# Kernel tuning notes

Hardware: AMD Instinct MI355X
Metric: run time of the kernel (lower is better)

Reference implementation:

```python
import jax, jax.numpy as jnp
import numpy as np

B, T, S, D = 8, 128, 512, 128  # batch, decoder steps, encoder len, output_dim==input_dim


def setup_inputs() -> dict:
    key = jax.random.key(0)
    ks = jax.random.split(key, 24)
    g = lambda i, shape: jax.random.normal(ks[i], shape, dtype=jnp.float32) * 0.05
    inp = {
        "x": g(0, (B, T, D)),
        "H": g(1, (B, S, D)),
        "init_states": jnp.zeros((2, B, D), jnp.float32),
        "Wa": g(2, (D, D)), "Ua": g(3, (D, D)), "v": g(4, (D,)),
        "Wi": g(5, (D, D)), "Ui": g(6, (D, D)), "Ci": g(7, (D, D)), "bi": jnp.zeros((D,), jnp.float32),
        "Wf": g(8, (D, D)), "Uf": g(9, (D, D)), "Cf": g(10, (D, D)), "bf": jnp.ones((D,), jnp.float32),
        "Wc": g(11, (D, D)), "Uc": g(12, (D, D)), "Cc": g(13, (D, D)), "bc": jnp.zeros((D,), jnp.float32),
        "Wo": g(14, (D, D)), "Uo": g(15, (D, D)), "Co": g(16, (D, D)), "bo": jnp.zeros((D,), jnp.float32),
    }
    return inp


def _forward(x, H, init_states, Wa, Ua, v, Wi, Ui, Ci, bi, Wf, Uf, Cf, bf,
             Wc, Uc, Cc, bc, Wo, Uo, Co, bo):
    # A = H @ Ua is loop-invariant in the original step(); hoist it (same math).
    HU = jnp.einsum('bsd,de->bse', H, Ua)  # [B,S,D]

    def step(carry, x_t):
        h_prev, c_prev = carry  # each [B,D]
        # Bahdanau attention over the full encoder sequence
        q = h_prev @ Wa                                        # [B,D]
        score = jnp.einsum('bsd,d->bs', jnp.tanh(HU + q[:, None, :]), v)  # [B,S]
        a = jax.nn.softmax(score, axis=-1)                     # [B,S]
        context = jnp.einsum('bsd,bs->bd', H, a)               # [B,D]
        # 4-gate LSTM update
        i_g = jax.nn.sigmoid(x_t @ Wi + h_prev @ Ui + context @ Ci + bi)
        f_g = jax.nn.sigmoid(x_t @ Wf + h_prev @ Uf + context @ Cf + bf)
        g_w = jnp.tanh(x_t @ Wc + h_prev @ Uc + context @ Cc + bc)
        c_t = f_g * c_prev + i_g * g_w
        o_g = jax.nn.sigmoid(x_t @ Wo + h_prev @ Uo + context @ Co + bo)
        h_t = o_g * jnp.tanh(c_t)
        return (h_t, c_t), h_t

    h0, c0 = init_states[0], init_states[1]
    x_tm = jnp.transpose(x, (1, 0, 2))  # time-major [T,B,D]
    _, hs = jax.lax.scan(step, (h0, c0), x_tm)  # hs: [T,B,D]
    return jnp.transpose(hs, (1, 0, 2))  # [B,T,D] hidden states (original returns [0] of stacked [h,c])


def reference(x, H, init_states, Wa, Ua, v, Wi, Ui, Ci, bi, Wf, Uf, Cf, bf,
              Wc, Uc, Cc, bc, Wo, Uo, Co, bo):
    return _forward(x, H, init_states, Wa, Ua, v, Wi, Ui, Ci, bi, Wf, Uf, Cf, bf,
                    Wc, Uc, Cc, bc, Wo, Uo, Co, bo)
```

## Files before the change

kernel.cpp:

```cpp
#include <hip/hip_runtime.h>

#define DEV __device__ __forceinline__

constexpr int nB = 8, nT = 128, nS = 512, nD = 128;
constexpr int J   = 4;
constexpr int SL  = 128;
constexpr int NTH = 512;

constexpr int S1_CNT = nB * J * 130;
constexpr int S2_OFF = S1_CNT;
constexpr int S2_CNT = nB * J * 32;
constexpr int XW_F   = (S1_CNT + S2_CNT) * 2;

DEV float tanh_small(float x) {
    float x2 = x * x;
    float p = fmaf(x2, 0.133333333f, -0.333333333f);
    return fmaf(x * x2, p, x);
}
DEV float fast_tanh(float x) {
    x = fminf(4.0f, fmaxf(-4.0f, x));
    float x2 = x * x;
    float num = fmaf(fmaf(x2 + 378.0f, x2, 17325.0f), x2, 135135.0f);
    float den = fmaf(fmaf(fmaf(x2, 28.0f, 3150.0f), x2, 62370.0f), x2, 135135.0f);
    return x * num * __builtin_amdgcn_rcpf(den);
}
DEV float fast_sig(float x) { return fmaf(fast_tanh(0.5f * x), 0.5f, 0.5f); }

typedef unsigned long long u64;
DEV u64  pk(float v, unsigned tag) { return ((u64)tag << 32) | (u64)__float_as_uint(v); }
DEV void st64(u64* p, u64 v) { __hip_atomic_store(p, v, __ATOMIC_RELAXED, __HIP_MEMORY_SCOPE_AGENT); }
DEV u64  ld64(const u64* p)  { return __hip_atomic_load(p, __ATOMIC_RELAXED, __HIP_MEMORY_SCOPE_AGENT); }
DEV float poll64(const u64* p, unsigned want) {
    for (;;) {
        u64 q = ld64(p);
        if ((unsigned)(q >> 32) == want) return __uint_as_float((unsigned)q);
        __builtin_amdgcn_s_sleep(1);
    }
}

__global__ void init_kernel(float* __restrict__ ws) {
    u64* p = (u64*)ws;
    for (int i = threadIdx.x; i < S1_CNT + S2_CNT; i += 1024)
        __hip_atomic_store(p + i, 0ull, __ATOMIC_RELAXED, __HIP_MEMORY_SCOPE_AGENT);
}

__global__ __launch_bounds__(NTH, 1) void attn_lstm_kernel(
    const float* __restrict__ x,  const float* __restrict__ H,
    const float* __restrict__ init_states, const float* __restrict__ Wa,
    const float* __restrict__ Ua, const float* __restrict__ v,
    const float* __restrict__ Wi, const float* __restrict__ Ui,
    const float* __restrict__ Ci, const float* __restrict__ bi,
    const float* __restrict__ Wf, const float* __restrict__ Uf,
    const float* __restrict__ Cf, const float* __restrict__ bf,
    const float* __restrict__ Wc, const float* __restrict__ Uc,
    const float* __restrict__ Cc, const float* __restrict__ bc,
    const float* __restrict__ Wo, const float* __restrict__ Uo,
    const float* __restrict__ Co, const float* __restrict__ bo,
    float* __restrict__ out, float* __restrict__ ws)
{
    const int tid = threadIdx.x;
    const int b = blockIdx.x & 7;
    const int j = blockIdx.x >> 3;

    u64*   S1   = (u64*)ws;
    u64*   S2   = (u64*)ws + S2_OFF;
    float* wsXW = ws + XW_F;

    __shared__ __align__(16) float Hs[SL * nD];
    __shared__ __align__(16) float q_l[nD];
    __shared__ __align__(16) float ctx_l[nD];
    __shared__ __align__(16) float h_l[nD];
    __shared__ __align__(16) float e_l[SL];
    __shared__ float pre_l[nD];
    __shared__ float pNx[3 * nD];
    __shared__ float mS_l[4];

    const int hi = tid >> 2, lo = tid & 3;
    const int g = hi >> 5, dd = hi & 31, gcol = 32 * j + dd;

    const float* Ug = (g == 0) ? Ui : (g == 1) ? Uf : (g == 2) ? Uc : Uo;
    const float* Cg = (g == 0) ? Ci : (g == 1) ? Cf : (g == 2) ? Cc : Co;
    const float* Bg = (g == 0) ? bi : (g == 1) ? bf : (g == 2) ? bc : bo;

    {
        for (int k = tid; k < 16384; k += NTH) {
            int gg = k >> 12, r = (k >> 5) & 127, i = k & 31;
            const float* Wm = (gg == 0) ? Wi : (gg == 1) ? Wf : (gg == 2) ? Wc : Wo;
            Hs[k] = Wm[r * nD + 32 * j + i];
        }
    }
    __syncthreads();

    {
        float acc[32];
        #pragma unroll
        for (int i = 0; i < 32; ++i) acc[i] = 0.0f;
        const float* xrow = x + ((size_t)b * nT + hi) * nD;
        for (int r = 0; r < nD; ++r) {
            float xr = xrow[r];
            const float* wrow = &Hs[lo * 4096 + r * 32];
            #pragma unroll
            for (int i = 0; i < 32; ++i) acc[i] = fmaf(xr, wrow[i], acc[i]);
        }
        float* dst = wsXW + ((size_t)(b * J + j) * nT + hi) * nD + lo * 32;
        #pragma unroll
        for (int k = 0; k < 8; ++k)
            ((float4*)dst)[k] = make_float4(acc[4*k], acc[4*k+1], acc[4*k+2], acc[4*k+3]);
    }
    __syncthreads();

    for (int k = tid; k < 16384; k += NTH) Hs[k] = Ua[k];
    __syncthreads();

    float HU_r[32];
    {
        #pragma unroll
        for (int i = 0; i < 32; ++i) HU_r[i] = 0.0f;
        const float* hrow = H + ((size_t)b * nS + (size_t)SL * j + hi) * nD;
        for (int r = 0; r < nD; ++r) {
            float hr = hrow[r];
            const float* uar = &Hs[r * nD + lo * 32];
            #pragma unroll
            for (int k = 0; k < 8; ++k) {
                int rk = (k + 2 * lo) & 7;
                #pragma unroll
                for (int m = 0; m < 4; ++m)
                    HU_r[4*k+m] = fmaf(hr, uar[rk * 4 + m], HU_r[4*k+m]);
            }
        }
    }
    __syncthreads();

    {
        const float* hrow = H + ((size_t)b * nS + (size_t)SL * j + hi) * nD + lo * 32;
        int c = hi >> 4, w = hi & 15;
        #pragma unroll
        for (int k = 0; k < 8; ++k) {
            float4 hv = ((const float4*)hrow)[k];
            int d0 = lo * 32 + 4 * k;
            Hs[(d0+0) * nD + ((c ^ ((d0+0) & 7)) * 16) + w] = hv.x;
            Hs[(d0+1) * nD + ((c ^ ((d0+1) & 7)) * 16) + w] = hv.y;
            Hs[(d0+2) * nD + ((c ^ ((d0+2) & 7)) * 16) + w] = hv.z;
            Hs[(d0+3) * nD + ((c ^ ((d0+3) & 7)) * 16) + w] = hv.w;
        }
    }

    float wa_r[32], u_r[32], c_r2[32], v_r[32];
    #pragma unroll
    for (int k = 0; k < 8; ++k) {
        int rk = (k + 2 * lo) & 7;
        #pragma unroll
        for (int m = 0; m < 4; ++m) {
            int row = lo * 32 + rk * 4 + m;
            wa_r[4*k+m] = Wa[row * nD + hi];
            u_r [4*k+m] = Ug[row * nD + gcol];
            c_r2[4*k+m] = Cg[row * nD + gcol];
            v_r [4*k+m] = v[row];
        }
    }
    const float bval = Bg[gcol];
    float c_reg = (tid < 32) ? init_states[nB * nD + b * nD + 32 * j + tid] : 0.0f;

    if (tid < nD) h_l[tid] = init_states[b * nD + tid];
    __syncthreads();

    u64* myN = S1 + (size_t)(b * J + j) * 130;
    u64* myH = S2 + (size_t)(b * J + j) * 32;

    for (int t = 0; t < nT; ++t) {
        const unsigned tg = (unsigned)(t + 1);

        float xwv = 0.0f;
        if (lo == 0) xwv = wsXW[((size_t)(b * J + j) * nT + t) * nD + hi];

        float qa = 0.0f, uasum = 0.0f;
        {
            const float4* h4 = (const float4*)h_l;
            #pragma unroll
            for (int k = 0; k < 8; ++k) {
                int rk = (k + 2 * lo) & 7;
                float4 hv = h4[lo * 8 + rk];
                qa    = fmaf(hv.x, wa_r[4*k+0], qa);
                qa    = fmaf(hv.y, wa_r[4*k+1], qa);
                qa    = fmaf(hv.z, wa_r[4*k+2], qa);
                qa    = fmaf(hv.w, wa_r[4*k+3], qa);
                uasum = fmaf(hv.x, u_r[4*k+0], uasum);
                uasum = fmaf(hv.y, u_r[4*k+1], uasum);
                uasum = fmaf(hv.z, u_r[4*k+2], uasum);
                uasum = fmaf(hv.w, u_r[4*k+3], uasum);
            }
        }
        qa += __shfl_xor(qa, 1);  qa += __shfl_xor(qa, 2);
        uasum += __shfl_xor(uasum, 1);  uasum += __shfl_xor(uasum, 2);
        if (lo == 0) q_l[hi] = qa;
        __syncthreads();

        float sa = 0.0f;
        {
            const float4* q4 = (const float4*)q_l;
            #pragma unroll
            for (int k = 0; k < 8; ++k) {
                int rk = (k + 2 * lo) & 7;
                float4 qq = q4[lo * 8 + rk];
                sa = fmaf(v_r[4*k+0], tanh_small(HU_r[4*k+0] + qq.x), sa);
                sa = fmaf(v_r[4*k+1], tanh_small(HU_r[4*k+1] + qq.y), sa);
                sa = fmaf(v_r[4*k+2], tanh_small(HU_r[4*k+2] + qq.z), sa);
                sa = fmaf(v_r[4*k+3], tanh_small(HU_r[4*k+3] + qq.w), sa);
            }
        }
        sa += __shfl_xor(sa, 1);  sa += __shfl_xor(sa, 2);
        if (lo == 0) e_l[hi] = __expf(sa);
        __syncthreads();

        float na = 0.0f, sea = 0.0f;
        #pragma unroll
        for (int cc = 0; cc < 2; ++cc) {
            int c = 2 * lo + cc;
            int pc = c ^ (hi & 7);
            const float4* hp = (const float4*)&Hs[hi * nD + pc * 16];
            const float4* ep = (const float4*)&e_l[c * 16];
            #pragma unroll
            for (int k2 = 0; k2 < 4; ++k2) {
                int kr = (k2 + lo) & 3;
                float4 hh = hp[kr]; float4 ee = ep[kr];
                na = fmaf(ee.x, hh.x, na); na = fmaf(ee.y, hh.y, na);
                na = fmaf(ee.z, hh.z, na); na = fmaf(ee.w, hh.w, na);
                sea += (ee.x + ee.y) + (ee.z + ee.w);
            }
        }
        na  += __shfl_xor(na, 1);   na  += __shfl_xor(na, 2);
        sea += __shfl_xor(sea, 1);  sea += __shfl_xor(sea, 2);

        if (lo == 0) st64(myN + hi, pk(na, tg));
        if (tid == 0) st64(myN + 128, pk(sea, tg));
        if (tid < 384) {
            int pi = tid >> 7, d2 = tid & 127;
            int jj = pi + (pi >= j);
            pNx[pi * nD + d2] = poll64(S1 + (size_t)(b * J + jj) * 130 + d2, tg);
        }
        if (tid >= 384 && tid < 387) {
            int pi = tid - 384;
            int jj = pi + (pi >= j);
            mS_l[pi] = poll64(S1 + (size_t)(b * J + jj) * 130 + 128, tg);
        }
        __syncthreads();

        if (lo == 0) {
            float nsum = na + pNx[hi] + pNx[nD + hi] + pNx[2 * nD + hi];
            float ssum = sea + mS_l[0] + mS_l[1] + mS_l[2];
            ctx_l[hi] = nsum * __builtin_amdgcn_rcpf(ssum);
        }
        __syncthreads();

        float ca = 0.0f;
        {
            const float4* cx4 = (const float4*)ctx_l;
            #pragma unroll
            for (int k = 0; k < 8; ++k) {
                int rk = (k + 2 * lo) & 7;
                float4 cv = cx4[lo * 8 + rk];
                ca = fmaf(cv.x, c_r2[4*k+0], ca);
                ca = fmaf(cv.y, c_r2[4*k+1], ca);
                ca = fmaf(cv.z, c_r2[4*k+2], ca);
                ca = fmaf(cv.w, c_r2[4*k+3], ca);
            }
        }
        ca += __shfl_xor(ca, 1);  ca += __shfl_xor(ca, 2);
        if (lo == 0) pre_l[hi] = uasum + ca + xwv + bval;
        __syncthreads();

        if (tid < 32) {
            float p_i = pre_l[tid], p_f = pre_l[32 + tid];
            float p_c = pre_l[64 + tid], p_o = pre_l[96 + tid];
            float ig = fast_sig(p_i), fg = fast_sig(p_f);
            float gg = fast_tanh(p_c), og = fast_sig(p_o);
            c_reg = fmaf(fg, c_reg, ig * gg);
            float hn = og * fast_tanh(c_reg);
            st64(myH + tid, pk(hn, tg));
            h_l[32 * j + tid] = hn;
            out[((size_t)b * nT + t) * nD + 32 * j + tid] = hn;
        }
        if (tid >= 32 && tid < 128) {
            int k = tid - 32, pi = k >> 5, dd2 = k & 31;
            int jj = pi + (pi >= j);
            h_l[32 * jj + dd2] = poll64(S2 + (size_t)(b * J + jj) * 32 + dd2, tg);
        }
        __syncthreads();
    }
}

extern "C" void kernel_launch(void* const* d_in, const int* in_sizes, int n_in,
                              void* d_out, int out_size, void* d_ws, size_t ws_size,
                              hipStream_t stream) {
    const float* x  = (const float*)d_in[0];
    const float* H  = (const float*)d_in[1];
    const float* is = (const float*)d_in[2];
    const float* Wa = (const float*)d_in[3];
    const float* Ua = (const float*)d_in[4];
    const float* v  = (const float*)d_in[5];
    const float* Wi = (const float*)d_in[6];
    const float* Ui = (const float*)d_in[7];
    const float* Ci = (const float*)d_in[8];
    const float* bi = (const float*)d_in[9];
    const float* Wf = (const float*)d_in[10];
    const float* Uf = (const float*)d_in[11];
    const float* Cf = (const float*)d_in[12];
    const float* bf = (const float*)d_in[13];
    const float* Wc = (const float*)d_in[14];
    const float* Uc = (const float*)d_in[15];
    const float* Cc = (const float*)d_in[16];
    const float* bc = (const float*)d_in[17];
    const float* Wo = (const float*)d_in[18];
    const float* Uo = (const float*)d_in[19];
    const float* Co = (const float*)d_in[20];
    const float* bo = (const float*)d_in[21];
    float* out = (float*)d_out;
    float* ws  = (float*)d_ws;

    hipLaunchKernelGGL(init_kernel, dim3(1), dim3(1024), 0, stream, ws);
    hipLaunchKernelGGL(attn_lstm_kernel, dim3(nB * J), dim3(NTH), 0, stream,
                       x, H, is, Wa, Ua, v,
                       Wi, Ui, Ci, bi, Wf, Uf, Cf, bf,
                       Wc, Uc, Cc, bc, Wo, Uo, Co, bo,
                       out, ws);
}
```

Baseline: 644.7 us.

## Interleave two batch elements per block to hide cross-block sync latency

```diff
diff --git a/kernel.cpp b/kernel.cpp
--- a/kernel.cpp
+++ b/kernel.cpp
@@ -6,6 +6,7 @@
 constexpr int J   = 4;
 constexpr int SL  = 128;
 constexpr int NTH = 512;
+constexpr int NP  = 4;
 
 constexpr int S1_CNT = nB * J * 130;
 constexpr int S2_OFF = S1_CNT;
@@ -43,6 +44,80 @@
     for (int i = threadIdx.x; i < S1_CNT + S2_CNT; i += 1024)
         __hip_atomic_store(p + i, 0ull, __ATOMIC_RELAXED, __HIP_MEMORY_SCOPE_AGENT);
 }
+
+#define PHASE_A(HLDS, QA, UA, QL) do {                                      \
+    QA = 0.0f; UA = 0.0f;                                                   \
+    const float4* h4_ = (const float4*)(HLDS);                              \
+    _Pragma("unroll")                                                       \
+    for (int k = 0; k < 8; ++k) {                                           \
+        int rk = (k + 2 * lo) & 7;                                          \
+        float4 hv = h4_[lo * 8 + rk];                                       \
+        QA = fmaf(hv.x, wa_r[4*k+0], QA);                                   \
+        QA = fmaf(hv.y, wa_r[4*k+1], QA);                                   \
+        QA = fmaf(hv.z, wa_r[4*k+2], QA);                                   \
+        QA = fmaf(hv.w, wa_r[4*k+3], QA);                                   \
+        UA = fmaf(hv.x, u_r[4*k+0], UA);                                    \
+        UA = fmaf(hv.y, u_r[4*k+1], UA);                                    \
+        UA = fmaf(hv.z, u_r[4*k+2], UA);                                    \
+        UA = fmaf(hv.w, u_r[4*k+3], UA);                                    \
+    }                                                                       \
+    QA += __shfl_xor(QA, 1);  QA += __shfl_xor(QA, 2);                      \
+    UA += __shfl_xor(UA, 1);  UA += __shfl_xor(UA, 2);                      \
+    if (lo == 0) (QL)[hi] = QA;                                             \
+} while (0)
+
+#define PHASE_C(HUR, QL, EL) do {                                           \
+    float sa_ = 0.0f;                                                       \
+    const float4* q4_ = (const float4*)(QL);                                \
+    _Pragma("unroll")                                                       \
+    for (int k = 0; k < 8; ++k) {                                           \
+        int rk = (k + 2 * lo) & 7;                                          \
+        float4 qq = q4_[lo * 8 + rk];                                       \
+        sa_ = fmaf(v_r[4*k+0], tanh_small(HUR[4*k+0] + qq.x), sa_);         \
+        sa_ = fmaf(v_r[4*k+1], tanh_small(HUR[4*k+1] + qq.y), sa_);         \
+        sa_ = fmaf(v_r[4*k+2], tanh_small(HUR[4*k+2] + qq.z), sa_);         \
+        sa_ = fmaf(v_r[4*k+3], tanh_small(HUR[4*k+3] + qq.w), sa_);         \
+    }                                                                       \
+    sa_ += __shfl_xor(sa_, 1);  sa_ += __shfl_xor(sa_, 2);                  \
+    if (lo == 0) (EL)[hi] = __expf(sa_);                                    \
+} while (0)
+
+#define PHASE_E(HSS, EL, NA, SEA) do {                                      \
+    NA = 0.0f; SEA = 0.0f;                                                  \
+    _Pragma("unroll")                                                       \
+    for (int cc = 0; cc < 2; ++cc) {                                        \
+        int c_ = 2 * lo + cc;                                               \
+        int pc_ = c_ ^ (hi & 7);                                            \
+        const float4* hp_ = (const float4*)&(HSS)[hi * nD + pc_ * 16];      \
+        const float4* ep_ = (const float4*)&(EL)[c_ * 16];                  \
+        _Pragma("unroll")                                                   \
+        for (int k2 = 0; k2 < 4; ++k2) {                                    \
+            int kr = (k2 + lo) & 3;                                         \
+            float4 hh = hp_[kr]; float4 ee = ep_[kr];                       \
+            NA = fmaf(ee.x, hh.x, NA); NA = fmaf(ee.y, hh.y, NA);           \
+            NA = fmaf(ee.z, hh.z, NA); NA = fmaf(ee.w, hh.w, NA);           \
+            SEA += (ee.x + ee.y) + (ee.z + ee.w);                           \
+        }                                                                   \
+    }                                                                       \
+    NA  += __shfl_xor(NA, 1);   NA  += __shfl_xor(NA, 2);                   \
+    SEA += __shfl_xor(SEA, 1);  SEA += __shfl_xor(SEA, 2);                  \
+} while (0)
+
+#define PHASE_H(CTX, UA, XWV, PREL) do {                                    \
+    float ca_ = 0.0f;                                                       \
+    const float4* cx4_ = (const float4*)(CTX);                              \
+    _Pragma("unroll")                                                       \
+    for (int k = 0; k < 8; ++k) {                                           \
+        int rk = (k + 2 * lo) & 7;                                          \
+        float4 cv = cx4_[lo * 8 + rk];                                      \
+        ca_ = fmaf(cv.x, c_r2[4*k+0], ca_);                                 \
+        ca_ = fmaf(cv.y, c_r2[4*k+1], ca_);                                 \
+        ca_ = fmaf(cv.z, c_r2[4*k+2], ca_);                                 \
+        ca_ = fmaf(cv.w, c_r2[4*k+3], ca_);                                 \
+    }                                                                       \
+    ca_ += __shfl_xor(ca_, 1);  ca_ += __shfl_xor(ca_, 2);                  \
+    if (lo == 0) (PREL)[hi] = (UA) + ca_ + (XWV);                           \
+} while (0)
 
 __global__ __launch_bounds__(NTH, 1) void attn_lstm_kernel(
     const float* __restrict__ x,  const float* __restrict__ H,
@@ -59,89 +134,102 @@
     float* __restrict__ out, float* __restrict__ ws)
 {
     const int tid = threadIdx.x;
-    const int b = blockIdx.x & 7;
-    const int j = blockIdx.x >> 3;
+    const int p = blockIdx.x & 3;
+    const int j = blockIdx.x >> 2;
+    const int b1 = 2 * p, b2 = 2 * p + 1;
 
     u64*   S1   = (u64*)ws;
     u64*   S2   = (u64*)ws + S2_OFF;
     float* wsXW = ws + XW_F;
 
-    __shared__ __align__(16) float Hs[SL * nD];
-    __shared__ __align__(16) float q_l[nD];
-    __shared__ __align__(16) float ctx_l[nD];
-    __shared__ __align__(16) float h_l[nD];
-    __shared__ __align__(16) float e_l[SL];
-    __shared__ float pre_l[nD];
-    __shared__ float pNx[3 * nD];
-    __shared__ float mS_l[4];
+    __shared__ __align__(16) float Hs1[SL * nD];
+    __shared__ __align__(16) float Hs2[SL * nD];
+    __shared__ __align__(16) float q_l[2][nD];
+    __shared__ __align__(16) float ctx_l[2][nD];
+    __shared__ __align__(16) float h_l[2][nD];
+    __shared__ __align__(16) float e_l[2][SL];
+    __shared__ __align__(16) float pre_l[2][nD];
+    __shared__ __align__(16) float pNx[2][3 * nD];
+    __shared__ float mS_l[2][4];
 
     const int hi = tid >> 2, lo = tid & 3;
     const int g = hi >> 5, dd = hi & 31, gcol = 32 * j + dd;
 
     const float* Ug = (g == 0) ? Ui : (g == 1) ? Uf : (g == 2) ? Uc : Uo;
     const float* Cg = (g == 0) ? Ci : (g == 1) ? Cf : (g == 2) ? Cc : Co;
-    const float* Bg = (g == 0) ? bi : (g == 1) ? bf : (g == 2) ? bc : bo;
-
-    {
-        for (int k = tid; k < 16384; k += NTH) {
-            int gg = k >> 12, r = (k >> 5) & 127, i = k & 31;
-            const float* Wm = (gg == 0) ? Wi : (gg == 1) ? Wf : (gg == 2) ? Wc : Wo;
-            Hs[k] = Wm[r * nD + 32 * j + i];
-        }
+
+    for (int k = tid; k < 16384; k += NTH) {
+        int gg = k >> 12, r = (k >> 5) & 127, i = k & 31;
+        const float* Wm = (gg == 0) ? Wi : (gg == 1) ? Wf : (gg == 2) ? Wc : Wo;
+        Hs1[k] = Wm[r * nD + 32 * j + i];
     }
     __syncthreads();
 
-    {
+    for (int s = 0; s < 2; ++s) {
+        const int bb = b1 + s;
         float acc[32];
         #pragma unroll
         for (int i = 0; i < 32; ++i) acc[i] = 0.0f;
-        const float* xrow = x + ((size_t)b * nT + hi) * nD;
+        const float* xrow = x + ((size_t)bb * nT + hi) * nD;
         for (int r = 0; r < nD; ++r) {
             float xr = xrow[r];
-            const float* wrow = &Hs[lo * 4096 + r * 32];
+            const float* wrow = &Hs1[lo * 4096 + r * 32];
             #pragma unroll
             for (int i = 0; i < 32; ++i) acc[i] = fmaf(xr, wrow[i], acc[i]);
         }
-        float* dst = wsXW + ((size_t)(b * J + j) * nT + hi) * nD + lo * 32;
+        const float* Bl = (lo == 0) ? bi : (lo == 1) ? bf : (lo == 2) ? bc : bo;
+        #pragma unroll
+        for (int i = 0; i < 32; ++i) acc[i] += Bl[32 * j + i];
+        float* dst = wsXW + ((size_t)(bb * J + j) * nT + hi) * nD + lo * 32;
         #pragma unroll
         for (int k = 0; k < 8; ++k)
             ((float4*)dst)[k] = make_float4(acc[4*k], acc[4*k+1], acc[4*k+2], acc[4*k+3]);
     }
     __syncthreads();
 
-    for (int k = tid; k < 16384; k += NTH) Hs[k] = Ua[k];
+    for (int k = tid; k < 16384; k += NTH) Hs1[k] = Ua[k];
     __syncthreads();
 
-    float HU_r[32];
+    float HU_r1[32], HU_r2[32];
     {
         #pragma unroll
-        for (int i = 0; i < 32; ++i) HU_r[i] = 0.0f;
-        const float* hrow = H + ((size_t)b * nS + (size_t)SL * j + hi) * nD;
+        for (int i = 0; i < 32; ++i) { HU_r1[i] = 0.0f; HU_r2[i] = 0.0f; }
+        const float* hrow1 = H + ((size_t)b1 * nS + (size_t)SL * j + hi) * nD;
+        const float* hrow2 = H + ((size_t)b2 * nS + (size_t)SL * j + hi) * nD;
         for (int r = 0; r < nD; ++r) {
-            float hr = hrow[r];
-            const float* uar = &Hs[r * nD + lo * 32];
+            float hr1 = hrow1[r], hr2 = hrow2[r];
+            const float* uar = &Hs1[r * nD + lo * 32];
             #pragma unroll
             for (int k = 0; k < 8; ++k) {
                 int rk = (k + 2 * lo) & 7;
                 #pragma unroll
-                for (int m = 0; m < 4; ++m)
-                    HU_r[4*k+m] = fmaf(hr, uar[rk * 4 + m], HU_r[4*k+m]);
+                for (int m = 0; m < 4; ++m) {
+                    float uv = uar[rk * 4 + m];
+                    HU_r1[4*k+m] = fmaf(hr1, uv, HU_r1[4*k+m]);
+                    HU_r2[4*k+m] = fmaf(hr2, uv, HU_r2[4*k+m]);
+                }
             }
         }
     }
     __syncthreads();
 
     {
-        const float* hrow = H + ((size_t)b * nS + (size_t)SL * j + hi) * nD + lo * 32;
+        const float* hr1 = H + ((size_t)b1 * nS + (size_t)SL * j + hi) * nD + lo * 32;
+        const float* hr2 = H + ((size_t)b2 * nS + (size_t)SL * j + hi) * nD + lo * 32;
         int c = hi >> 4, w = hi & 15;
         #pragma unroll
         for (int k = 0; k < 8; ++k) {
-            float4 hv = ((const float4*)hrow)[k];
+            float4 v1 = ((const float4*)hr1)[k];
+            float4 v2 = ((const float4*)hr2)[k];
             int d0 = lo * 32 + 4 * k;
-            Hs[(d0+0) * nD + ((c ^ ((d0+0) & 7)) * 16) + w] = hv.x;
-            Hs[(d0+1) * nD + ((c ^ ((d0+1) & 7)) * 16) + w] = hv.y;
-            Hs[(d0+2) * nD + ((c ^ ((d0+2) & 7)) * 16) + w] = hv.z;
-            Hs[(d0+3) * nD + ((c ^ ((d0+3) & 7)) * 16) + w] = hv.w;
+            Hs1[(d0+0) * nD + ((c ^ ((d0+0) & 7)) * 16) + w] = v1.x;
+            Hs1[(d0+1) * nD + ((c ^ ((d0+1) & 7)) * 16) + w] = v1.y;
+            Hs1[(d0+2) * nD + ((c ^ ((d0+2) & 7)) * 16) + w] = v1.z;
+            Hs1[(d0+3) * nD + ((c ^ ((d0+3) & 7)) * 16) + w] = v1.w;
+            Hs2[(d0+0) * nD + ((c ^ ((d0+0) & 7)) * 16) + w] = v2.x;
+            Hs2[(d0+1) * nD + ((c ^ ((d0+1) & 7)) * 16) + w] = v2.y;
+            Hs2[(d0+2) * nD + ((c ^ ((d0+2) & 7)) * 16) + w] = v2.z;
+            Hs2[(d0+3) * nD + ((c ^ ((d0+3) & 7)) * 16) + w] = v2.w;
         }
     }
 
@@ -158,132 +246,126 @@
             v_r [4*k+m] = v[row];
         }
     }
-    const float bval = Bg[gcol];
-    float c_reg = (tid < 32) ? init_states[nB * nD + b * nD + 32 * j + tid] : 0.0f;
-
-    if (tid < nD) h_l[tid] = init_states[b * nD + tid];
+    float c1_reg = (tid < 32) ? init_states[nB * nD + b1 * nD + 32 * j + tid] : 0.0f;
+    float c2_reg = (tid < 32) ? init_states[nB * nD + b2 * nD + 32 * j + tid] : 0.0f;
+
+    if (tid < nD) {
+        h_l[0][tid] = init_states[b1 * nD + tid];
+        h_l[1][tid] = init_states[b2 * nD + tid];
+    }
     __syncthreads();
 
-    u64* myN = S1 + (size_t)(b * J + j) * 130;
-    u64* myH = S2 + (size_t)(b * J + j) * 32;
+    u64* myN1 = S1 + (size_t)(b1 * J + j) * 130;
+    u64* myN2 = S1 + (size_t)(b2 * J + j) * 130;
+    u64* myH1 = S2 + (size_t)(b1 * J + j) * 32;
+    u64* myH2 = S2 + (size_t)(b2 * J + j) * 32;
 
     for (int t = 0; t < nT; ++t) {
         const unsigned tg = (unsigned)(t + 1);
 
-        float xwv = 0.0f;
-        if (lo == 0) xwv = wsXW[((size_t)(b * J + j) * nT + t) * nD + hi];
-
-        float qa = 0.0f, uasum = 0.0f;
-        {
-            const float4* h4 = (const float4*)h_l;
-            #pragma unroll
-            for (int k = 0; k < 8; ++k) {
-                int rk = (k + 2 * lo) & 7;
-                float4 hv = h4[lo * 8 + rk];
-                qa    = fmaf(hv.x, wa_r[4*k+0], qa);
-                qa    = fmaf(hv.y, wa_r[4*k+1], qa);
-                qa    = fmaf(hv.z, wa_r[4*k+2], qa);
-                qa    = fmaf(hv.w, wa_r[4*k+3], qa);
-                uasum = fmaf(hv.x, u_r[4*k+0], uasum);
-                uasum = fmaf(hv.y, u_r[4*k+1], uasum);
-                uasum = fmaf(hv.z, u_r[4*k+2], uasum);
-                uasum = fmaf(hv.w, u_r[4*k+3], uasum);
+        float xwv1 = 0.0f, xwv2 = 0.0f;
+        if (lo == 0) {
+            xwv1 = wsXW[((size_t)(b1 * J + j) * nT + t) * nD + hi];
+            xwv2 = wsXW[((size_t)(b2 * J + j) * nT + t) * nD + hi];
+        }
+
+        float qa1, ua1;
+        PHASE_A(h_l[0], qa1, ua1, q_l[0]);
+        __syncthreads();
+        PHASE_C(HU_r1, q_l[0], e_l[0]);
+        __syncthreads();
+        float na1, se1;
+        PHASE_E(Hs1, e_l[0], na1, se1);
+        if (lo == 0) st64(myN1 + hi, pk(na1, tg));
+        if (tid == 0) st64(myN1 + 128, pk(se1, tg));
+
+        if (t > 0) {
+            if (tid >= 32 && tid < 128) {
+                int k = tid - 32, pi = k >> 5, dd2 = k & 31;
+                int jj = pi + (pi >= j);
+                h_l[1][32 * jj + dd2] = poll64(S2 + (size_t)(b2 * J + jj) * 32 + dd2, (unsigned)t);
             }
         }
-        qa += __shfl_xor(qa, 1);  qa += __shfl_xor(qa, 2);
-        uasum += __shfl_xor(uasum, 1);  uasum += __shfl_xor(uasum, 2);
-        if (lo == 0) q_l[hi] = qa;
-        __syncthreads();
-
-        float sa = 0.0f;
-        {
-            const float4* q4 = (const float4*)q_l;
-            #pragma unroll
-            for (int k = 0; k < 8; ++k) {
-                int rk = (k + 2 * lo) & 7;
-                float4 qq = q4[lo * 8 + rk];
-                sa = fmaf(v_r[4*k+0], tanh_small(HU_r[4*k+0] + qq.x), sa);
-                sa = fmaf(v_r[4*k+1], tanh_small(HU_r[4*k+1] + qq.y), sa);
-                sa = fmaf(v_r[4*k+2], tanh_small(HU_r[4*k+2] + qq.z), sa);
-                sa = fmaf(v_r[4*k+3], tanh_small(HU_r[4*k+3] + qq.w), sa);
-            }
-        }
-        sa += __shfl_xor(sa, 1);  sa += __shfl_xor(sa, 2);
-        if (lo == 0) e_l[hi] = __expf(sa);
-        __syncthreads();
-
-        float na = 0.0f, sea = 0.0f;
-        #pragma unroll
-        for (int cc = 0; cc < 2; ++cc) {
-            int c = 2 * lo + cc;
-            int pc = c ^ (hi & 7);
-            const float4* hp = (const float4*)&Hs[hi * nD + pc * 16];
-            const float4* ep = (const float4*)&e_l[c * 16];
-            #pragma unroll
-            for (int k2 = 0; k2 < 4; ++k2) {
-                int kr = (k2 + lo) & 3;
-                float4 hh = hp[kr]; float4 ee = ep[kr];
-                na = fmaf(ee.x, hh.x, na); na = fmaf(ee.y, hh.y, na);
-                na = fmaf(ee.z, hh.z, na); na = fmaf(ee.w, hh.w, na);
-                sea += (ee.x + ee.y) + (ee.z + ee.w);
-            }
-        }
-        na  += __shfl_xor(na, 1);   na  += __shfl_xor(na, 2);
-        sea += __shfl_xor(sea, 1);  sea += __shfl_xor(sea, 2);
-
-        if (lo == 0) st64(myN + hi, pk(na, tg));
-        if (tid == 0) st64(myN + 128, pk(sea, tg));
+        __syncthreads();
+
+        float qa2, ua2;
+        PHASE_A(h_l[1], qa2, ua2, q_l[1]);
+        __syncthreads();
+        PHASE_C(HU_r2, q_l[1], e_l[1]);
+        __syncthreads();
+        float na2, se2;
+        PHASE_E(Hs2, e_l[1], na2, se2);
+        if (lo == 0) st64(myN2 + hi, pk(na2, tg));
+        if (tid == 0) st64(myN2 + 128, pk(se2, tg));
+
         if (tid < 384) {
             int pi = tid >> 7, d2 = tid & 127;
             int jj = pi + (pi >= j);
-            pNx[pi * nD + d2] = poll64(S1 + (size_t)(b * J + jj) * 130 + d2, tg);
+            pNx[0][pi * nD + d2] = poll64(S1 + (size_t)(b1 * J + jj) * 130 + d2, tg);
         }
         if (tid >= 384 && tid < 387) {
             int pi = tid - 384;
             int jj = pi + (pi >= j);
-            mS_l[pi] = poll64(S1 + (size_t)(b * J + jj) * 130 + 128, tg);
+            mS_l[0][pi] = poll64(S1 + (size_t)(b1 * J + jj) * 130 + 128, tg);
         }
         __syncthreads();
 
         if (lo == 0) {
-            float nsum = na + pNx[hi] + pNx[nD + hi] + pNx[2 * nD + hi];
-            float ssum = sea + mS_l[0] + mS_l[1] + mS_l[2];
-            ctx_l[hi] = nsum * __builtin_amdgcn_rcpf(ssum);
-        }
-        __syncthreads();
-
-        float ca = 0.0f;
-        {
-            const float4* cx4 = (const float4*)ctx_l;
-            #pragma unroll
-            for (int k = 0; k < 8; ++k) {
-                int rk = (k + 2 * lo) & 7;
-                float4 cv = cx4[lo * 8 + rk];
-                ca = fmaf(cv.x, c_r2[4*k+0], ca);
-                ca = fmaf(cv.y, c_r2[4*k+1], ca);
-                ca = fmaf(cv.z, c_r2[4*k+2], ca);
-                ca = fmaf(cv.w, c_r2[4*k+3], ca);
-            }
-        }
-        ca += __shfl_xor(ca, 1);  ca += __shfl_xor(ca, 2);
-        if (lo == 0) pre_l[hi] = uasum + ca + xwv + bval;
-        __syncthreads();
-
+            float nsum = na1 + pNx[0][hi] + pNx[0][nD + hi] + pNx[0][2 * nD + hi];
+            float ssum = se1 + mS_l[0][0] + mS_l[0][1] + mS_l[0][2];
+            ctx_l[0][hi] = nsum * __builtin_amdgcn_rcpf(ssum);
+        }
+        __syncthreads();
+        PHASE_H(ctx_l[0], ua1, xwv1, pre_l[0]);
+        __syncthreads();
         if (tid < 32) {
-            float p_i = pre_l[tid], p_f = pre_l[32 + tid];
-            float p_c = pre_l[64 + tid], p_o = pre_l[96 + tid];
+            float p_i = pre_l[0][tid],      p_f = pre_l[0][32 + tid];
+            float p_c = pre_l[0][64 + tid], p_o = pre_l[0][96 + tid];
             float ig = fast_sig(p_i), fg = fast_sig(p_f);
             float gg = fast_tanh(p_c), og = fast_sig(p_o);
-            c_reg = fmaf(fg, c_reg, ig * gg);
-            float hn = og * fast_tanh(c_reg);
-            st64(myH + tid, pk(hn, tg));
-            h_l[32 * j + tid] = hn;
-            out[((size_t)b * nT + t) * nD + 32 * j + tid] = hn;
-        }
+            c1_reg = fmaf(fg, c1_reg, ig * gg);
+            float hn = og * fast_tanh(c1_reg);
+            st64(myH1 + tid, pk(hn, tg));
+            h_l[0][32 * j + tid] = hn;
+            out[((size_t)b1 * nT + t) * nD + 32 * j + tid] = hn;
+        }
+
+        if (tid < 384) {
+            int pi = tid >> 7, d2 = tid & 127;
+            int jj = pi + (pi >= j);
+            pNx[1][pi * nD + d2] = poll64(S1 + (size_t)(b2 * J + jj) * 130 + d2, tg);
+        }
+        if (tid >= 384 && tid < 387) {
+            int pi = tid - 384;
+            int jj = pi + (pi >= j);
+            mS_l[1][pi] = poll64(S1 + (size_t)(b2 * J + jj) * 130 + 128, tg);
+        }
+        __syncthreads();
+
+        if (lo == 0) {
+            float nsum = na2 + pNx[1][hi] + pNx[1][nD + hi] + pNx[1][2 * nD + hi];
+            float ssum = se2 + mS_l[1][0] + mS_l[1][1] + mS_l[1][2];
+            ctx_l[1][hi] = nsum * __builtin_amdgcn_rcpf(ssum);
+        }
+        __syncthreads();
+        PHASE_H(ctx_l[1], ua2, xwv2, pre_l[1]);
+        __syncthreads();
+        if (tid < 32) {
+            float p_i = pre_l[1][tid],      p_f = pre_l[1][32 + tid];
+            float p_c = pre_l[1][64 + tid], p_o = pre_l[1][96 + tid];
+            float ig = fast_sig(p_i), fg = fast_sig(p_f);
+            float gg = fast_tanh(p_c), og = fast_sig(p_o);
+            c2_reg = fmaf(fg, c2_reg, ig * gg);
+            float hn = og * fast_tanh(c2_reg);
+            st64(myH2 + tid, pk(hn, tg));
+            h_l[1][32 * j + tid] = hn;
+            out[((size_t)b2 * nT + t) * nD + 32 * j + tid] = hn;
+        }
+
         if (tid >= 32 && tid < 128) {
             int k = tid - 32, pi = k >> 5, dd2 = k & 31;
             int jj = pi + (pi >= j);
-            h_l[32 * jj + dd2] = poll64(S2 + (size_t)(b * J + jj) * 32 + dd2, tg);
+            h_l[0][32 * jj + dd2] = poll64(S2 + (size_t)(b1 * J + jj) * 32 + dd2, tg);
         }
         __syncthreads();
     }
@@ -318,7 +400,7 @@
     float* ws  = (float*)d_ws;
 
     hipLaunchKernelGGL(init_kernel, dim3(1), dim3(1024), 0, stream, ws);
-    hipLaunchKernelGGL(attn_lstm_kernel, dim3(nB * J), dim3(NTH), 0, stream,
+    hipLaunchKernelGGL(attn_lstm_kernel, dim3(NP * J), dim3(NTH), 0, stream,
                        x, H, is, Wa, Ua, v,
                        Wi, Ui, Ci, bi, Wf, Uf, Cf, bf,
                        Wc, Uc, Cc, bc, Wo, Uo, Co, bo,
```

After: 1.702 ms. +164.1%, slower.

## Interleave gate rows per lane and drop shared-memory staging barriers

Applied to the files above, without the earlier changes.

```diff
diff --git a/kernel.cpp b/kernel.cpp
--- a/kernel.cpp
+++ b/kernel.cpp
@@ -71,12 +71,9 @@
     __shared__ __align__(16) float ctx_l[nD];
     __shared__ __align__(16) float h_l[nD];
     __shared__ __align__(16) float e_l[SL];
-    __shared__ float pre_l[nD];
-    __shared__ float pNx[3 * nD];
-    __shared__ float mS_l[4];
 
     const int hi = tid >> 2, lo = tid & 3;
-    const int g = hi >> 5, dd = hi & 31, gcol = 32 * j + dd;
+    const int g = hi & 3, dd = hi >> 2, gcol = 32 * j + dd;
 
     const float* Ug = (g == 0) ? Ui : (g == 1) ? Uf : (g == 2) ? Uc : Uo;
     const float* Cg = (g == 0) ? Ci : (g == 1) ? Cf : (g == 2) ? Cc : Co;
@@ -159,19 +156,24 @@
         }
     }
     const float bval = Bg[gcol];
-    float c_reg = (tid < 32) ? init_states[nB * nD + b * nD + 32 * j + tid] : 0.0f;
+    float c_reg = ((tid & 15) == 0)
+        ? init_states[nB * nD + b * nD + 32 * j + (tid >> 4)] : 0.0f;
 
     if (tid < nD) h_l[tid] = init_states[b * nD + tid];
     __syncthreads();
 
     u64* myN = S1 + (size_t)(b * J + j) * 130;
     u64* myH = S2 + (size_t)(b * J + j) * 32;
+    const int jj0 = 0 + (0 >= j), jj1 = 1 + (1 >= j), jj2 = 2 + (2 >= j);
+    const u64* pN0 = S1 + (size_t)(b * J + jj0) * 130;
+    const u64* pN1 = S1 + (size_t)(b * J + jj1) * 130;
+    const u64* pN2 = S1 + (size_t)(b * J + jj2) * 130;
 
     for (int t = 0; t < nT; ++t) {
         const unsigned tg = (unsigned)(t + 1);
 
         float xwv = 0.0f;
-        if (lo == 0) xwv = wsXW[((size_t)(b * J + j) * nT + t) * nD + hi];
+        if (lo == 0) xwv = wsXW[((size_t)(b * J + j) * nT + t) * nD + (g * 32 + dd)];
 
         float qa = 0.0f, uasum = 0.0f;
         {
@@ -233,21 +235,22 @@
 
         if (lo == 0) st64(myN + hi, pk(na, tg));
         if (tid == 0) st64(myN + 128, pk(sea, tg));
-        if (tid < 384) {
-            int pi = tid >> 7, d2 = tid & 127;
-            int jj = pi + (pi >= j);
-            pNx[pi * nD + d2] = poll64(S1 + (size_t)(b * J + jj) * 130 + d2, tg);
-        }
-        if (tid >= 384 && tid < 387) {
-            int pi = tid - 384;
-            int jj = pi + (pi >= j);
-            mS_l[pi] = poll64(S1 + (size_t)(b * J + jj) * 130 + 128, tg);
-        }
-        __syncthreads();
-
         if (lo == 0) {
-            float nsum = na + pNx[hi] + pNx[nD + hi] + pNx[2 * nD + hi];
-            float ssum = sea + mS_l[0] + mS_l[1] + mS_l[2];
+            u64 a0, a1, a2, s0, s1, s2;
+            for (;;) {
+                a0 = ld64(pN0 + hi);  a1 = ld64(pN1 + hi);  a2 = ld64(pN2 + hi);
+                s0 = ld64(pN0 + 128); s1 = ld64(pN1 + 128); s2 = ld64(pN2 + 128);
+                if ((unsigned)(a0 >> 32) == tg && (unsigned)(a1 >> 32) == tg &&
+                    (unsigned)(a2 >> 32) == tg && (unsigned)(s0 >> 32) == tg &&
+                    (unsigned)(s1 >> 32) == tg && (unsigned)(s2 >> 32) == tg) break;
+                __builtin_amdgcn_s_sleep(1);
+            }
+            float nsum = na + __uint_as_float((unsigned)a0)
+                            + __uint_as_float((unsigned)a1)
+                            + __uint_as_float((unsigned)a2);
+            float ssum = sea + __uint_as_float((unsigned)s0)
+                             + __uint_as_float((unsigned)s1)
+                             + __uint_as_float((unsigned)s2);
             ctx_l[hi] = nsum * __builtin_amdgcn_rcpf(ssum);
         }
         __syncthreads();
@@ -266,19 +269,20 @@
             }
         }
         ca += __shfl_xor(ca, 1);  ca += __shfl_xor(ca, 2);
-        if (lo == 0) pre_l[hi] = uasum + ca + xwv + bval;
-        __syncthreads();
-
-        if (tid < 32) {
-            float p_i = pre_l[tid], p_f = pre_l[32 + tid];
-            float p_c = pre_l[64 + tid], p_o = pre_l[96 + tid];
-            float ig = fast_sig(p_i), fg = fast_sig(p_f);
-            float gg = fast_tanh(p_c), og = fast_sig(p_o);
-            c_reg = fmaf(fg, c_reg, ig * gg);
+        float pre = uasum + ca + xwv + bval;
+        float p_f = __shfl_down(pre, 4);
+        float p_c = __shfl_down(pre, 8);
+        float p_o = __shfl_down(pre, 12);
+
+        if ((tid & 15) == 0) {
+            int ddl = tid >> 4;
+            float ig = fast_sig(pre), fg = fast_sig(p_f);
+            float gg2 = fast_tanh(p_c), og = fast_sig(p_o);
+            c_reg = fmaf(fg, c_reg, ig * gg2);
             float hn = og * fast_tanh(c_reg);
-            st64(myH + tid, pk(hn, tg));
-            h_l[32 * j + tid] = hn;
-            out[((size_t)b * nT + t) * nD + 32 * j + tid] = hn;
+            st64(myH + ddl, pk(hn, tg));
+            h_l[32 * j + ddl] = hn;
+            out[((size_t)b * nT + t) * nD + 32 * j + ddl] = hn;
         }
         if (tid >= 32 && tid < 128) {
             int k = tid - 32, pi = k >> 5, dd2 = k & 31;
```

Result: slower. 736.7 us (+14.3%).
